# Kernel optimization log

Hardware: AMD Instinct MI355X
Metric: run time of the kernel (lower is better)

The kernel has to match this reference:

```python
import jax, jax.numpy as jnp
import numpy as np
from jax import lax

N, E, F, H, B = 16384, 262144, 32, 128, 16
DI, DS, DC, DTR = 256, 16, 4, 8   # Mamba: d_inner=expand*H, d_state, d_conv, dt_rank=ceil(H/16)
NS, NC = 512, 8                   # num_stations, num line colors
EPS = 1e-5


def _forward(node_features, edge_index, batch, W_in, b_in, W_g1, b_g1, W_g2, b_g2,
             W_inproj, conv_w, conv_b, W_xproj, W_dt, b_dt, A_log, D_p, W_out,
             gamma, beta, Wc, bc, Wh, bh, Wt, bt, Wp1, bp1, Wp2, bp2, Wd, bd, Ws, bs):
    def gcn(x, W, b):
        # GCNConv with self-loops and symmetric normalization
        loops = jnp.arange(N)
        s = jnp.concatenate([edge_index[0], loops])
        d = jnp.concatenate([edge_index[1], loops])
        deg = jax.ops.segment_sum(jnp.ones(s.shape[0], x.dtype), d, num_segments=N)
        dinv = jnp.where(deg > 0, lax.rsqrt(deg), 0.0)
        xw = x @ W
        msg = xw[s] * (dinv[s] * dinv[d])[:, None]
        return jax.ops.segment_sum(msg, d, num_segments=N) + b

    h = jax.nn.relu(node_features @ W_in + b_in)
    h = jax.nn.relu(gcn(h, W_g1, b_g1))
    h_gnn = jax.nn.relu(gcn(h, W_g2, b_g2))

    # --- Mamba block over the node sequence (batch dim of 1, seq_len = N) ---
    xz = h_gnn @ W_inproj                      # (N, 2*DI)
    x, z = xz[:, :DI], xz[:, DI:]
    xp = jnp.pad(x, ((DC - 1, 0), (0, 0)))     # causal depthwise conv1d
    xc = conv_b + sum(xp[k:k + N] * conv_w[:, k] for k in range(DC))
    x = jax.nn.silu(xc)
    dbl = x @ W_xproj                          # (N, DTR + 2*DS)
    dt = jax.nn.softplus(dbl[:, :DTR] @ W_dt + b_dt)   # (N, DI)
    Bm = dbl[:, DTR:DTR + DS]                  # (N, DS)
    Cm = dbl[:, DTR + DS:]                     # (N, DS)
    A = -jnp.exp(A_log)                        # (DI, DS)
    dA = jnp.exp(dt[:, :, None] * A[None])     # (N, DI, DS)
    dBx = dt[:, :, None] * Bm[:, None, :] * x[:, :, None]

    def step(hst, t):
        dA_t, dBx_t, C_t = t
        hst = dA_t * hst + dBx_t               # (DI, DS)
        return hst, hst @ C_t                  # (DI,)

    _, ys = lax.scan(step, jnp.zeros((DI, DS), x.dtype), (dA, dBx, Cm))
    y = (ys + D_p * x) * jax.nn.silu(z)
    h_mamba = y @ W_out                        # (N, H)

    # residual + LayerNorm
    hh = h_gnn + h_mamba
    mu = hh.mean(-1, keepdims=True)
    var = ((hh - mu) ** 2).mean(-1, keepdims=True)
    h_final = (hh - mu) * lax.rsqrt(var + EPS) * gamma + beta

    # global_mean_pool per graph
    counts = jax.ops.segment_sum(jnp.ones(N, h_final.dtype), batch, num_segments=B)
    ge = jax.ops.segment_sum(h_final, batch, num_segments=B) / jnp.maximum(counts, 1.0)[:, None]

    # critic + all policy heads, concatenated: [1,4,3,NS,NS,NS,NC]
    return jnp.concatenate([ge @ Wc + bc, ge @ Wh + bh, ge @ Wt + bt,
                            ge @ Wp1 + bp1, ge @ Wp2 + bp2, ge @ Wd + bd,
                            ge @ Ws + bs], axis=-1)


def setup_inputs() -> dict:
    key = jax.random.key(0)
    ks = list(jax.random.split(key, 20))
    p = lambda i, shape, s=0.02: jax.random.normal(ks[i], shape, jnp.float32) * s
    return dict(
        node_features=jax.random.normal(ks[0], (N, F), jnp.float32),
        edge_index=jax.random.randint(ks[1], (2, E), 0, N),
        batch=jnp.sort(jax.random.randint(ks[2], (N,), 0, B)),
        W_in=p(3, (F, H)), b_in=jnp.zeros((H,), jnp.float32),
        W_g1=p(4, (H, H)), b_g1=jnp.zeros((H,), jnp.float32),
        W_g2=p(5, (H, H)), b_g2=jnp.zeros((H,), jnp.float32),
        W_inproj=p(6, (H, 2 * DI)),
        conv_w=p(7, (DI, DC)), conv_b=jnp.zeros((DI,), jnp.float32),
        W_xproj=p(8, (DI, DTR + 2 * DS)),
        W_dt=p(9, (DTR, DI)), b_dt=jnp.full((DI,), -4.0, jnp.float32),
        A_log=jnp.log(jnp.broadcast_to(jnp.arange(1.0, DS + 1.0, dtype=jnp.float32), (DI, DS))),
        D_p=jnp.ones((DI,), jnp.float32),
        W_out=p(10, (DI, H)),
        gamma=jnp.ones((H,), jnp.float32), beta=jnp.zeros((H,), jnp.float32),
        Wc=p(11, (H, 1)), bc=jnp.zeros((1,), jnp.float32),
        Wh=p(12, (H, 4)), bh=jnp.zeros((4,), jnp.float32),
        Wt=p(13, (H, 3)), bt=jnp.zeros((3,), jnp.float32),
        Wp1=p(14, (H, NS)), bp1=jnp.zeros((NS,), jnp.float32),
        Wp2=p(15, (H, NS)), bp2=jnp.zeros((NS,), jnp.float32),
        Wd=p(16, (H, NS)), bd=jnp.zeros((NS,), jnp.float32),
        Ws=p(17, (H, NC)), bs=jnp.zeros((NC,), jnp.float32),
    )


def reference(node_features, edge_index, batch, W_in, b_in, W_g1, b_g1, W_g2, b_g2,
              W_inproj, conv_w, conv_b, W_xproj, W_dt, b_dt, A_log, D_p, W_out,
              gamma, beta, Wc, bc, Wh, bh, Wt, bt, Wp1, bp1, Wp2, bp2, Wd, bd, Ws, bs):
    return _forward(node_features, edge_index, batch, W_in, b_in, W_g1, b_g1, W_g2, b_g2,
                    W_inproj, conv_w, conv_b, W_xproj, W_dt, b_dt, A_log, D_p, W_out,
                    gamma, beta, Wc, bc, Wh, bh, Wt, bt, Wp1, bp1, Wp2, bp2, Wd, bd, Ws, bs)
```

## Files before the change

kernel.cpp:

```cpp
#include <hip/hip_runtime.h>
#include <math.h>

#define NN 16384
#define EE 262144
#define FF 32
#define HH 128
#define BB 16
#define DI 256
#define DS 16
#define DC 4
#define DTR 8
#define OUTW 1552
#define NCH 256
#define CHLEN 64
#define NG 8
#define GL 32

__device__ __forceinline__ float siluf(float v) { return v / (1.f + __expf(-v)); }
__device__ __forceinline__ float softplusf(float v) {
    return fmaxf(v, 0.f) + __logf(1.f + __expf(-fabsf(v)));
}

__global__ void deg_kernel(const int* __restrict__ dst, int* __restrict__ cnt) {
    int e = blockIdx.x * blockDim.x + threadIdx.x;
    if (e < EE) atomicAdd(&cnt[dst[e]], 1);
}

__global__ __launch_bounds__(1024) void prefix_kernel(const int* __restrict__ cnt,
                                                      int* __restrict__ rowptr,
                                                      int* __restrict__ cursor,
                                                      float* __restrict__ dinv) {
    __shared__ int part[1024];
    int tid = threadIdx.x;
    int4 c4[4];
#pragma unroll
    for (int j = 0; j < 4; j++) c4[j] = ((const int4*)cnt)[tid * 4 + j];
    int v[16] = {c4[0].x, c4[0].y, c4[0].z, c4[0].w, c4[1].x, c4[1].y, c4[1].z, c4[1].w,
                 c4[2].x, c4[2].y, c4[2].z, c4[2].w, c4[3].x, c4[3].y, c4[3].z, c4[3].w};
    int s = 0;
#pragma unroll
    for (int j = 0; j < 16; j++) s += v[j];
    part[tid] = s;
    __syncthreads();
    for (int off = 1; off < 1024; off <<= 1) {
        int t = (tid >= off) ? part[tid - off] : 0;
        __syncthreads();
        part[tid] += t;
        __syncthreads();
    }
    int running = part[tid] - s;
    int rp[16];
    float dv[16];
#pragma unroll
    for (int j = 0; j < 16; j++) {
        rp[j] = running;
        running += v[j];
        dv[j] = rsqrtf((float)(v[j] + 1));
    }
#pragma unroll
    for (int j = 0; j < 4; j++) {
        int4 r4; r4.x = rp[j*4]; r4.y = rp[j*4+1]; r4.z = rp[j*4+2]; r4.w = rp[j*4+3];
        ((int4*)rowptr)[tid * 4 + j] = r4;
        ((int4*)cursor)[tid * 4 + j] = r4;
        float4 d4; d4.x = dv[j*4]; d4.y = dv[j*4+1]; d4.z = dv[j*4+2]; d4.w = dv[j*4+3];
        ((float4*)dinv)[tid * 4 + j] = d4;
    }
    if (tid == 1023) rowptr[NN] = part[1023];
}

__global__ void scatter_kernel(const int* __restrict__ src, const int* __restrict__ dst,
                               int* __restrict__ cursor, int* __restrict__ col) {
    int e = blockIdx.x * blockDim.x + threadIdx.x;
    if (e < EE) {
        int d = dst[e];
        int pos = atomicAdd(&cursor[d], 1);
        col[pos] = src[e];
    }
}

__global__ __launch_bounds__(256) void gemm_k(const float* __restrict__ A,
                                              const float* __restrict__ B,
                                              const float* __restrict__ bias,
                                              float* __restrict__ C,
                                              int M, int Nn, int K, int act) {
    __shared__ float As[16][68];
    __shared__ float Bs[16][68];
    int tid = threadIdx.x;
    int m0 = blockIdx.y * 64;
    int n0 = blockIdx.x * 64;
    int ty = tid >> 4, tx = tid & 15;
    float acc[4][4] = {{0.f}};
    for (int k0 = 0; k0 < K; k0 += 16) {
#pragma unroll
        for (int l = 0; l < 4; l++) {
            int idx = tid + l * 256;
            int i = idx >> 4, j = idx & 15;
            As[j][i] = A[(size_t)(m0 + i) * K + k0 + j];
        }
#pragma unroll
        for (int l = 0; l < 4; l++) {
            int idx = tid + l * 256;
            int i = idx >> 6, j = idx & 63;
            int n = n0 + j;
            Bs[i][j] = (n < Nn) ? B[(size_t)(k0 + i) * Nn + n] : 0.f;
        }
        __syncthreads();
#pragma unroll
        for (int kk = 0; kk < 16; kk++) {
            float4 a4 = *(const float4*)&As[kk][ty * 4];
            float4 b4 = *(const float4*)&Bs[kk][tx * 4];
            float av[4] = {a4.x, a4.y, a4.z, a4.w};
            float bv[4] = {b4.x, b4.y, b4.z, b4.w};
#pragma unroll
            for (int r = 0; r < 4; r++)
#pragma unroll
                for (int c = 0; c < 4; c++) acc[r][c] = fmaf(av[r], bv[c], acc[r][c]);
        }
        __syncthreads();
    }
    int nb = n0 + tx * 4;
    if (nb < Nn) {
        float4 bi4 = {0.f, 0.f, 0.f, 0.f};
        if (bias) bi4 = *(const float4*)&bias[nb];
#pragma unroll
        for (int r = 0; r < 4; r++) {
            int m = m0 + ty * 4 + r;
            float4 v;
            v.x = acc[r][0] + bi4.x; v.y = acc[r][1] + bi4.y;
            v.z = acc[r][2] + bi4.z; v.w = acc[r][3] + bi4.w;
            if (act == 1) {
                v.x = fmaxf(v.x, 0.f); v.y = fmaxf(v.y, 0.f);
                v.z = fmaxf(v.z, 0.f); v.w = fmaxf(v.w, 0.f);
            }
            *(float4*)&C[(size_t)m * Nn + nb] = v;
        }
    }
}

__global__ __launch_bounds__(256, 2) void gemm_big(const float* __restrict__ A,
                                                   const float* __restrict__ B,
                                                   float* __restrict__ C,
                                                   int M, int Nn, int K) {
    __shared__ float As[16][132];
    __shared__ float Bs[16][132];
    int tid = threadIdx.x;
    int m0 = blockIdx.y * 128;
    int n0 = blockIdx.x * 128;
    int ty = tid >> 4, tx = tid & 15;
    float acc[8][8] = {{0.f}};
    for (int k0 = 0; k0 < K; k0 += 16) {
        {
            int m = tid >> 1;
            int kc = (tid & 1) * 8;
            const float* ap = &A[(size_t)(m0 + m) * K + k0 + kc];
            float4 a0 = *(const float4*)ap;
            float4 a1 = *(const float4*)(ap + 4);
            As[kc + 0][m] = a0.x; As[kc + 1][m] = a0.y;
            As[kc + 2][m] = a0.z; As[kc + 3][m] = a0.w;
            As[kc + 4][m] = a1.x; As[kc + 5][m] = a1.y;
            As[kc + 6][m] = a1.z; As[kc + 7][m] = a1.w;
        }
        {
            int krow = tid >> 4;
            int c8 = (tid & 15) * 8;
            const float* bp = &B[(size_t)(k0 + krow) * Nn + n0 + c8];
            *(float4*)&Bs[krow][c8] = *(const float4*)bp;
            *(float4*)&Bs[krow][c8 + 4] = *(const float4*)(bp + 4);
        }
        __syncthreads();
#pragma unroll
        for (int kk = 0; kk < 16; kk++) {
            float4 a0 = *(const float4*)&As[kk][ty * 4];
            float4 a1 = *(const float4*)&As[kk][64 + ty * 4];
            float4 b0 = *(const float4*)&Bs[kk][tx * 4];
            float4 b1 = *(const float4*)&Bs[kk][64 + tx * 4];
            float av[8] = {a0.x, a0.y, a0.z, a0.w, a1.x, a1.y, a1.z, a1.w};
            float bv[8] = {b0.x, b0.y, b0.z, b0.w, b1.x, b1.y, b1.z, b1.w};
#pragma unroll
            for (int r = 0; r < 8; r++)
#pragma unroll
                for (int c = 0; c < 8; c++) acc[r][c] = fmaf(av[r], bv[c], acc[r][c]);
        }
        __syncthreads();
    }
#pragma unroll
    for (int r = 0; r < 8; r++) {
        int m = m0 + ((r < 4) ? (ty * 4 + r) : (64 + ty * 4 + r - 4));
        float4 v0, v1;
        v0.x = acc[r][0]; v0.y = acc[r][1]; v0.z = acc[r][2]; v0.w = acc[r][3];
        v1.x = acc[r][4]; v1.y = acc[r][5]; v1.z = acc[r][6]; v1.w = acc[r][7];
        *(float4*)&C[(size_t)m * Nn + n0 + tx * 4] = v0;
        *(float4*)&C[(size_t)m * Nn + n0 + 64 + tx * 4] = v1;
    }
}

__global__ __launch_bounds__(256) void gemm_at(const float* __restrict__ AT,
                                               const float* __restrict__ B,
                                               float* __restrict__ C,
                                               int M, int Nn, int K) {
    __shared__ float As[16][68];
    __shared__ float Bs[16][68];
    int tid = threadIdx.x;
    int m0 = blockIdx.y * 64;
    int n0 = blockIdx.x * 64;
    int ty = tid >> 4, tx = tid & 15;
    float acc[4][4] = {{0.f}};
    for (int k0 = 0; k0 < K; k0 += 16) {
#pragma unroll
        for (int l = 0; l < 4; l++) {
            int idx = tid + l * 256;
            int kk = idx >> 6, i = idx & 63;
            As[kk][i] = AT[(size_t)(k0 + kk) * M + m0 + i];
        }
#pragma unroll
        for (int l = 0; l < 4; l++) {
            int idx = tid + l * 256;
            int i = idx >> 6, j = idx & 63;
            int n = n0 + j;
            Bs[i][j] = (n < Nn) ? B[(size_t)(k0 + i) * Nn + n] : 0.f;
        }
        __syncthreads();
#pragma unroll
        for (int kk = 0; kk < 16; kk++) {
            float4 a4 = *(const float4*)&As[kk][ty * 4];
            float4 b4 = *(const float4*)&Bs[kk][tx * 4];
            float av[4] = {a4.x, a4.y, a4.z, a4.w};
            float bv[4] = {b4.x, b4.y, b4.z, b4.w};
#pragma unroll
            for (int r = 0; r < 4; r++)
#pragma unroll
                for (int c = 0; c < 4; c++) acc[r][c] = fmaf(av[r], bv[c], acc[r][c]);
        }
        __syncthreads();
    }
    int nb = n0 + tx * 4;
    if (nb < Nn) {
#pragma unroll
        for (int r = 0; r < 4; r++) {
            int m = m0 + ty * 4 + r;
            float4 v;
            v.x = acc[r][0]; v.y = acc[r][1]; v.z = acc[r][2]; v.w = acc[r][3];
            *(float4*)&C[(size_t)m * Nn + nb] = v;
        }
    }
}

__global__ void gcn_gather(const float* __restrict__ xw, const int* __restrict__ rowptr,
                           const int* __restrict__ col, const float* __restrict__ dinv,
                           const float* __restrict__ b, float* __restrict__ out) {
    int n = blockIdx.x;
    int f = threadIdx.x;
    float dn = dinv[n];
    float acc = xw[(size_t)n * HH + f] * dn * dn;
    int beg = rowptr[n], end = rowptr[n + 1];
    int e = beg;
    for (; e + 4 <= end; e += 4) {
        int s0 = col[e], s1 = col[e + 1], s2 = col[e + 2], s3 = col[e + 3];
        float w0 = dinv[s0] * dn, w1 = dinv[s1] * dn, w2 = dinv[s2] * dn, w3 = dinv[s3] * dn;
        float v0 = xw[(size_t)s0 * HH + f];
        float v1 = xw[(size_t)s1 * HH + f];
        float v2 = xw[(size_t)s2 * HH + f];
        float v3 = xw[(size_t)s3 * HH + f];
        acc = fmaf(v0, w0, acc);
        acc = fmaf(v1, w1, acc);
        acc = fmaf(v2, w2, acc);
        acc = fmaf(v3, w3, acc);
    }
    for (; e < end; e++) {
        int s0 = col[e];
        acc = fmaf(xw[(size_t)s0 * HH + f], dinv[s0] * dn, acc);
    }
    acc += b[f];
    out[(size_t)n * HH + f] = fmaxf(acc, 0.f);
}

__global__ __launch_bounds__(256) void conv_silu_t(const float* __restrict__ xz,
                                                   const float* __restrict__ cw,
                                                   const float* __restrict__ cb,
                                                   float* __restrict__ xst,
                                                   float* __restrict__ szt) {
    __shared__ float tile[67][65];
    int tid = threadIdx.x;
    int t0 = blockIdx.x * 64;
    int c0 = blockIdx.y * 64;
#pragma unroll
    for (int l = 0; l < 17; l++) {
        int idx = tid + l * 256;
        if (idx < 67 * 64) {
            int r = idx >> 6, c = idx & 63;
            int gt = t0 - 3 + r;
            tile[r][c] = (gt >= 0) ? xz[(size_t)gt * 512 + c0 + c] : 0.f;
        }
    }
    __syncthreads();
    int tl = tid & 63;
    int d0 = tid >> 6;
    if (c0 < 256) {
#pragma unroll
        for (int l = 0; l < 16; l++) {
            int dl = d0 + l * 4;
            int dg = c0 + dl;
            float acc = cb[dg];
#pragma unroll
            for (int k = 0; k < DC; k++)
                acc = fmaf(tile[tl + k][dl], cw[dg * DC + k], acc);
            xst[dg * NN + t0 + tl] = siluf(acc);
        }
    } else {
#pragma unroll
        for (int l = 0; l < 16; l++) {
            int dl = d0 + l * 4;
            int dg = c0 - 256 + dl;
            szt[dg * NN + t0 + tl] = siluf(tile[tl + 3][dl]);
        }
    }
}

__global__ __launch_bounds__(256) void transpose_dbl(const float* __restrict__ dbl,
                                                     float* __restrict__ dblt) {
    __shared__ float tile[64][41];
    int tid = threadIdx.x;
    int t0 = blockIdx.x * 64;
#pragma unroll
    for (int l = 0; l < 10; l++) {
        int idx = tid + l * 256;
        int r = idx / 40, c = idx - r * 40;
        tile[r][c] = dbl[(size_t)(t0 + r) * 40 + c];
    }
    __syncthreads();
#pragma unroll
    for (int l = 0; l < 10; l++) {
        int idx = tid + l * 256;
        int c = idx >> 6, t = idx & 63;
        dblt[c * NN + t0 + t] = tile[t][c];
    }
}

__global__ __launch_bounds__(256, 6) void scan_phase1(const float* __restrict__ xst,
                                                      const float* __restrict__ dblt,
                                                      const float* __restrict__ A_log,
                                                      const float* __restrict__ W_dt,
                                                      const float* __restrict__ b_dt,
                                                      float* __restrict__ chkP,
                                                      float* __restrict__ chkH) {
    __shared__ float Td[32][68];
    __shared__ float Tx[32][68];
    __shared__ float Bs[16][68];
    __shared__ float D8[8][68];
    int tid = threadIdx.x;
    int wave = tid >> 6, lane = tid & 63;
    int sg = lane & 7, dl = lane >> 3;
    int dblk = blockIdx.x, chunk = blockIdx.y;
    int t0 = chunk * CHLEN;
    int dloc = wave * 8 + dl;
    int d = dblk * 32 + dloc;
    int s0 = 2 * sg;
#pragma unroll
    for (int p = 0; p < 2; p++) {
        int linear = tid + p * 256;
        int row = linear >> 4, c4 = (linear & 15) * 4;
        *(float4*)&Tx[row][c4] = *(const float4*)&xst[(size_t)(dblk * 32 + row) * NN + t0 + c4];
    }
    if (tid < 128) {
        int r = tid >> 4, c4 = (tid & 15) * 4;
        *(float4*)&D8[r][c4] = *(const float4*)&dblt[(size_t)r * NN + t0 + c4];
    }
    {
        int s = tid >> 4, c4 = (tid & 15) * 4;
        *(float4*)&Bs[s][c4] = *(const float4*)&dblt[(size_t)(8 + s) * NN + t0 + c4];
    }
    float A0 = -expf(A_log[d * DS + s0]);
    float A1 = -expf(A_log[d * DS + s0 + 1]);
    __syncthreads();
    {
        int row = tid >> 3;
        int tb = (tid & 7) * 8;
        int dd = dblk * 32 + row;
        float bd = b_dt[dd];
        float wv[8];
#pragma unroll
        for (int j = 0; j < 8; j++) wv[j] = W_dt[j * DI + dd];
#pragma unroll
        for (int j = 0; j < 8; j++) {
            int t = tb + j;
            float acc = bd;
#pragma unroll
            for (int k = 0; k < 8; k++) acc = fmaf(D8[k][t], wv[k], acc);
            Td[row][t] = softplusf(acc);
        }
    }
    __syncthreads();
    float h0 = 0.f, h1 = 0.f, P0 = 1.f, P1 = 1.f;
    for (int i = 0; i < CHLEN; i += 4) {
        float4 d4 = *(const float4*)&Td[dloc][i];
        float4 x4 = *(const float4*)&Tx[dloc][i];
        float4 b04 = *(const float4*)&Bs[s0][i];
        float4 b14 = *(const float4*)&Bs[s0 + 1][i];
#define P1S(U) { float dtv = d4.U; float a0 = __expf(dtv * A0); float a1 = __expf(dtv * A1); \
        float dx = dtv * x4.U; h0 = fmaf(a0, h0, dx * b04.U); h1 = fmaf(a1, h1, dx * b14.U); \
        P0 *= a0; P1 *= a1; }
        P1S(x) P1S(y) P1S(z) P1S(w)
#undef P1S
    }
    int idx = chunk * 4096 + d * DS + s0;
    float2 vP; vP.x = P0; vP.y = P1;
    float2 vH; vH.x = h0; vH.y = h1;
    *(float2*)(chkP + idx) = vP;
    *(float2*)(chkH + idx) = vH;
}

__global__ void scan_phase2a(const float* __restrict__ chkP, const float* __restrict__ chkH,
                             float* __restrict__ gp, float* __restrict__ gh) {
    int g = blockIdx.x * blockDim.x + threadIdx.x;
    int idx = g & 4095;
    int grp = g >> 12;
    int c0 = grp * GL;
    float P = 1.f, H = 0.f;
    for (int j = 0; j < GL; j += 4) {
        float p[4], q[4];
#pragma unroll
        for (int jj = 0; jj < 4; jj++) {
            p[jj] = chkP[(c0 + j + jj) * 4096 + idx];
            q[jj] = chkH[(c0 + j + jj) * 4096 + idx];
        }
#pragma unroll
        for (int jj = 0; jj < 4; jj++) {
            H = fmaf(p[jj], H, q[jj]);
            P *= p[jj];
        }
    }
    gp[grp * 4096 + idx] = P;
    gh[grp * 4096 + idx] = H;
}

__global__ void scan_phase2b(const float* __restrict__ gp, const float* __restrict__ gh,
                             float* __restrict__ gini) {
    int idx = blockIdx.x * blockDim.x + threadIdx.x;
    float h = 0.f;
#pragma unroll
    for (int g = 0; g < NG; g++) {
        gini[g * 4096 + idx] = h;
        h = fmaf(gp[g * 4096 + idx], h, gh[g * 4096 + idx]);
    }
}

__global__ void scan_phase2c(const float* __restrict__ chkP, const float* __restrict__ chkH,
                             const float* __restrict__ gini, float* __restrict__ init) {
    int g = blockIdx.x * blockDim.x + threadIdx.x;
    int idx = g & 4095;
    int grp = g >> 12;
    int c0 = grp * GL;
    float h = gini[grp * 4096 + idx];
    for (int j = 0; j < GL; j += 4) {
        float p[4], q[4];
#pragma unroll
        for (int jj = 0; jj < 4; jj++) {
            p[jj] = chkP[(c0 + j + jj) * 4096 + idx];
            q[jj] = chkH[(c0 + j + jj) * 4096 + idx];
        }
#pragma unroll
        for (int jj = 0; jj < 4; jj++) {
            init[(c0 + j + jj) * 4096 + idx] = h;
            h = fmaf(p[jj], h, q[jj]);
        }
    }
}

__global__ __launch_bounds__(256, 5) void scan_phase3(const float* __restrict__ xst,
                                                      const float* __restrict__ dblt,
                                                      const float* __restrict__ A_log,
                                                      const float* __restrict__ W_dt,
                                                      const float* __restrict__ b_dt,
                                                      const float* __restrict__ init,
                                                      const float* __restrict__ D_p,
                                                      const float* __restrict__ szt,
                                                      float* __restrict__ yt) {
    __shared__ float Td[32][68];
    __shared__ float Tx[32][68];
    __shared__ float Bs[16][68];
    __shared__ float Cs[16][68];
    __shared__ float D8[8][68];
    int tid = threadIdx.x;
    int wave = tid >> 6, lane = tid & 63;
    int sg = lane & 7, dl = lane >> 3;
    int dblk = blockIdx.x, chunk = blockIdx.y;
    int t0 = chunk * CHLEN;
    int dloc = wave * 8 + dl;
    int d = dblk * 32 + dloc;
    int s0 = 2 * sg;
#pragma unroll
    for (int p = 0; p < 2; p++) {
        int linear = tid + p * 256;
        int row = linear >> 4, c4 = (linear & 15) * 4;
        *(float4*)&Tx[row][c4] = *(const float4*)&xst[(size_t)(dblk * 32 + row) * NN + t0 + c4];
    }
    if (tid < 128) {
        int r = tid >> 4, c4 = (tid & 15) * 4;
        *(float4*)&D8[r][c4] = *(const float4*)&dblt[(size_t)r * NN + t0 + c4];
    }
    {
        int s = tid >> 4, c4 = (tid & 15) * 4;
        *(float4*)&Bs[s][c4] = *(const float4*)&dblt[(size_t)(8 + s) * NN + t0 + c4];
        *(float4*)&Cs[s][c4] = *(const float4*)&dblt[(size_t)(24 + s) * NN + t0 + c4];
    }
    float A0 = -expf(A_log[d * DS + s0]);
    float A1 = -expf(A_log[d * DS + s0 + 1]);
    float Dd = D_p[d];
    float2 ini = *(const float2*)(init + chunk * 4096 + d * DS + s0);
    float h0 = ini.x, h1 = ini.y;
    __syncthreads();
    {
        int row = tid >> 3;
        int tb = (tid & 7) * 8;
        int dd = dblk * 32 + row;
        float bd = b_dt[dd];
        float wv[8];
#pragma unroll
        for (int j = 0; j < 8; j++) wv[j] = W_dt[j * DI + dd];
#pragma unroll
        for (int j = 0; j < 8; j++) {
            int t = tb + j;
            float acc = bd;
#pragma unroll
            for (int k = 0; k < 8; k++) acc = fmaf(D8[k][t], wv[k], acc);
            Td[row][t] = softplusf(acc);
        }
    }
    __syncthreads();
    for (int i = 0; i < CHLEN; i += 4) {
        float4 d4 = *(const float4*)&Td[dloc][i];
        float4 x4 = *(const float4*)&Tx[dloc][i];
        float4 b04 = *(const float4*)&Bs[s0][i];
        float4 b14 = *(const float4*)&Bs[s0 + 1][i];
        float4 c04 = *(const float4*)&Cs[s0][i];
        float4 c14 = *(const float4*)&Cs[s0 + 1][i];
        float4 yv;
#define P3S(U) { float dtv = d4.U; float a0 = __expf(dtv * A0); float a1 = __expf(dtv * A1); \
        float dx = dtv * x4.U; h0 = fmaf(a0, h0, dx * b04.U); h1 = fmaf(a1, h1, dx * b14.U); \
        float c = fmaf(h1, c14.U, h0 * c04.U); \
        c += __shfl_xor(c, 1); c += __shfl_xor(c, 2); c += __shfl_xor(c, 4); \
        yv.U = c + Dd * x4.U; }
        P3S(x) P3S(y) P3S(z) P3S(w)
#undef P3S
        if (sg == 0) *(float4*)&Td[dloc][i] = yv;
    }
#pragma unroll
    for (int r = 0; r < 8; r++) {
        int row = wave * 8 + r;
        float sz = szt[(size_t)(dblk * 32 + row) * NN + t0 + lane];
        yt[(size_t)(dblk * 32 + row) * NN + t0 + lane] = Td[row][lane] * sz;
    }
}

__global__ void add_ln(const float* __restrict__ hg, const float* __restrict__ hm,
                       const float* __restrict__ gamma, const float* __restrict__ beta,
                       float* __restrict__ out) {
    int row = blockIdx.x * 4 + (threadIdx.x >> 6);
    int lane = threadIdx.x & 63;
    size_t base = (size_t)row * HH;
    float v0 = hg[base + lane] + hm[base + lane];
    float v1 = hg[base + 64 + lane] + hm[base + 64 + lane];
    float sum = v0 + v1;
#pragma unroll
    for (int m = 32; m >= 1; m >>= 1) sum += __shfl_xor(sum, m);
    float mu = sum * (1.f / 128.f);
    float d0 = v0 - mu, d1 = v1 - mu;
    float vs = d0 * d0 + d1 * d1;
#pragma unroll
    for (int m = 32; m >= 1; m >>= 1) vs += __shfl_xor(vs, m);
    float inv = rsqrtf(vs * (1.f / 128.f) + 1e-5f);
    out[base + lane] = d0 * inv * gamma[lane] + beta[lane];
    out[base + 64 + lane] = d1 * inv * gamma[64 + lane] + beta[64 + lane];
}

__global__ void pool_kernel(const float* __restrict__ hf, const int* __restrict__ batch,
                            float* __restrict__ ge, int* __restrict__ counts) {
    int f = threadIdx.x;
    int r0 = blockIdx.x * 128;
    int gcur = batch[r0];
    float acc = 0.f;
    int cnt = 0;
    for (int i = 0; i < 128; i += 4) {
        int r = r0 + i;
        int g0 = batch[r], g3 = batch[r + 3];
        float v0 = hf[(size_t)r * HH + f];
        float v1 = hf[(size_t)(r + 1) * HH + f];
        float v2 = hf[(size_t)(r + 2) * HH + f];
        float v3 = hf[(size_t)(r + 3) * HH + f];
        if (g0 == gcur && g3 == gcur) {
            acc += (v0 + v1) + (v2 + v3);
            cnt += 4;
        } else {
            int gs[4] = {g0, batch[r + 1], batch[r + 2], g3};
            float vs[4] = {v0, v1, v2, v3};
#pragma unroll
            for (int k = 0; k < 4; k++) {
                if (gs[k] != gcur) {
                    atomicAdd(&ge[gcur * HH + f], acc);
                    if (f == 0) atomicAdd(&counts[gcur], cnt);
                    acc = 0.f; cnt = 0; gcur = gs[k];
                }
                acc += vs[k];
                cnt++;
            }
        }
    }
    atomicAdd(&ge[gcur * HH + f], acc);
    if (f == 0) atomicAdd(&counts[gcur], cnt);
}

__global__ void ge_norm(float* __restrict__ ge, const int* __restrict__ counts) {
    int idx = blockIdx.x * blockDim.x + threadIdx.x;
    if (idx < BB * HH) {
        int b = idx >> 7;
        ge[idx] /= fmaxf((float)counts[b], 1.f);
    }
}

__global__ void heads_kernel(const float* __restrict__ ge,
                             const float* Wc, const float* bc, const float* Wh, const float* bh,
                             const float* Wt, const float* bt, const float* Wp1, const float* bp1,
                             const float* Wp2, const float* bp2, const float* Wd, const float* bd,
                             const float* Ws, const float* bs, float* __restrict__ out) {
    int col = blockIdx.x * blockDim.x + threadIdx.x;
    int b = blockIdx.y;
    if (col >= OUTW) return;
    const float* W; const float* bi; int lc, w;
    if (col < 1)         { W = Wc;  bi = bc;  lc = col;        w = 1; }
    else if (col < 5)    { W = Wh;  bi = bh;  lc = col - 1;    w = 4; }
    else if (col < 8)    { W = Wt;  bi = bt;  lc = col - 5;    w = 3; }
    else if (col < 520)  { W = Wp1; bi = bp1; lc = col - 8;    w = 512; }
    else if (col < 1032) { W = Wp2; bi = bp2; lc = col - 520;  w = 512; }
    else if (col < 1544) { W = Wd;  bi = bd;  lc = col - 1032; w = 512; }
    else                 { W = Ws;  bi = bs;  lc = col - 1544; w = 8; }
    float acc = bi[lc];
#pragma unroll 8
    for (int f = 0; f < HH; f++) acc = fmaf(ge[b * HH + f], W[f * w + lc], acc);
    out[(size_t)b * OUTW + col] = acc;
}

extern "C" void kernel_launch(void* const* d_in, const int* in_sizes, int n_in,
                              void* d_out, int out_size, void* d_ws, size_t ws_size,
                              hipStream_t stream) {
    const float* nf      = (const float*)d_in[0];
    const int*   ei      = (const int*)d_in[1];
    const int*   batch   = (const int*)d_in[2];
    const float* W_in    = (const float*)d_in[3];
    const float* b_in    = (const float*)d_in[4];
    const float* W_g1    = (const float*)d_in[5];
    const float* b_g1    = (const float*)d_in[6];
    const float* W_g2    = (const float*)d_in[7];
    const float* b_g2    = (const float*)d_in[8];
    const float* W_inproj= (const float*)d_in[9];
    const float* conv_w  = (const float*)d_in[10];
    const float* conv_b  = (const float*)d_in[11];
    const float* W_xproj = (const float*)d_in[12];
    const float* W_dt    = (const float*)d_in[13];
    const float* b_dt    = (const float*)d_in[14];
    const float* A_log   = (const float*)d_in[15];
    const float* D_p     = (const float*)d_in[16];
    const float* W_out   = (const float*)d_in[17];
    const float* gamma   = (const float*)d_in[18];
    const float* beta    = (const float*)d_in[19];
    const float* Wc = (const float*)d_in[20]; const float* bc = (const float*)d_in[21];
    const float* Wh = (const float*)d_in[22]; const float* bh = (const float*)d_in[23];
    const float* Wt = (const float*)d_in[24]; const float* bt = (const float*)d_in[25];
    const float* Wp1= (const float*)d_in[26]; const float* bp1= (const float*)d_in[27];
    const float* Wp2= (const float*)d_in[28]; const float* bp2= (const float*)d_in[29];
    const float* Wd = (const float*)d_in[30]; const float* bd = (const float*)d_in[31];
    const float* Ws = (const float*)d_in[32]; const float* bs = (const float*)d_in[33];

    const int* e_src = ei;
    const int* e_dst = ei + EE;

    float* w = (float*)d_ws;
    size_t o = 0;
    float* F0   = w + o; o += (size_t)NN * HH;
    float* F1   = w + o; o += (size_t)NN * HH;
    float* F2   = w + o; o += (size_t)NN * HH;
    float* XZ   = w + o; o += (size_t)NN * 512;
    float* YT   = XZ;
    float* XST  = w + o; o += (size_t)NN * DI;
    float* SZT  = w + o; o += (size_t)NN * DI;
    float* DBL  = w + o; o += (size_t)NN * 40;
    float* DBLT = w + o; o += (size_t)NN * 40;
    float* GE   = w + o; o += BB * HH;
    float* DINV = w + o; o += NN;
    int* ip = (int*)(w + o);
    int* CNT    = ip; ip += NN;
    int* ROWPTR = ip; ip += NN + 1;
    int* CURSOR = ip; ip += NN;
    int* COL    = ip; ip += EE;
    int* COUNTS = ip; ip += BB;

    float* CHP  = F0;
    float* CHH  = F0 + (size_t)NCH * 4096;
    float* INI  = F1;
    float* GP   = DBL;
    float* GH   = DBL + NG * 4096;
    float* GINI = DBL + 2 * NG * 4096;

    hipMemsetAsync(CNT, 0, NN * sizeof(int), stream);
    hipMemsetAsync(GE, 0, BB * HH * sizeof(float), stream);
    hipMemsetAsync(COUNTS, 0, BB * sizeof(int), stream);

    deg_kernel<<<EE / 256, 256, 0, stream>>>(e_dst, CNT);
    prefix_kernel<<<1, 1024, 0, stream>>>(CNT, ROWPTR, CURSOR, DINV);
    scatter_kernel<<<EE / 256, 256, 0, stream>>>(e_src, e_dst, CURSOR, COL);

    gemm_k<<<dim3(2, NN / 64), 256, 0, stream>>>(nf, W_in, b_in, F0, NN, HH, FF, 1);
    gemm_k<<<dim3(2, NN / 64), 256, 0, stream>>>(F0, W_g1, nullptr, F1, NN, HH, HH, 0);
    gcn_gather<<<NN, HH, 0, stream>>>(F1, ROWPTR, COL, DINV, b_g1, F0);
    gemm_k<<<dim3(2, NN / 64), 256, 0, stream>>>(F0, W_g2, nullptr, F1, NN, HH, HH, 0);
    gcn_gather<<<NN, HH, 0, stream>>>(F1, ROWPTR, COL, DINV, b_g2, F2);

    gemm_big<<<dim3(4, NN / 128), 256, 0, stream>>>(F2, W_inproj, XZ, NN, 512, HH);
    conv_silu_t<<<dim3(NN / 64, 8), 256, 0, stream>>>(XZ, conv_w, conv_b, XST, SZT);
    gemm_at<<<dim3(1, NN / 64), 256, 0, stream>>>(XST, W_xproj, DBL, NN, 40, DI);
    transpose_dbl<<<NN / 64, 256, 0, stream>>>(DBL, DBLT);

    scan_phase1<<<dim3(8, NCH), 256, 0, stream>>>(XST, DBLT, A_log, W_dt, b_dt, CHP, CHH);
    scan_phase2a<<<(4096 * NG) / 256, 256, 0, stream>>>(CHP, CHH, GP, GH);
    scan_phase2b<<<16, 256, 0, stream>>>(GP, GH, GINI);
    scan_phase2c<<<(4096 * NG) / 256, 256, 0, stream>>>(CHP, CHH, GINI, INI);
    scan_phase3<<<dim3(8, NCH), 256, 0, stream>>>(XST, DBLT, A_log, W_dt, b_dt, INI, D_p, SZT, YT);

    gemm_at<<<dim3(2, NN / 64), 256, 0, stream>>>(YT, W_out, F1, NN, HH, DI);
    add_ln<<<NN / 4, 256, 0, stream>>>(F2, F1, gamma, beta, F0);

    pool_kernel<<<NN / 128, HH, 0, stream>>>(F0, batch, GE, COUNTS);
    ge_norm<<<(BB * HH + 255) / 256, 256, 0, stream>>>(GE, COUNTS);

    heads_kernel<<<dim3((OUTW + 127) / 128, BB), 128, 0, stream>>>(
        GE, Wc, bc, Wh, bh, Wt, bt, Wp1, bp1, Wp2, bp2, Wd, bd, Ws, bs, (float*)d_out);
}
```

Before: 449.0 us.

## Fuse out-proj GEMM with residual LayerNorm, vectorize GCN gather, fold pool normalization

```diff
diff --git a/kernel.cpp b/kernel.cpp
--- a/kernel.cpp
+++ b/kernel.cpp
@@ -137,7 +137,7 @@
     }
 }
 
-__global__ __launch_bounds__(256, 2) void gemm_big(const float* __restrict__ A,
+__global__ __launch_bounds__(256, 4) void gemm_big(const float* __restrict__ A,
                                                    const float* __restrict__ B,
                                                    float* __restrict__ C,
                                                    int M, int Nn, int K) {
@@ -245,33 +245,126 @@
     }
 }
 
-__global__ void gcn_gather(const float* __restrict__ xw, const int* __restrict__ rowptr,
-                           const int* __restrict__ col, const float* __restrict__ dinv,
-                           const float* __restrict__ b, float* __restrict__ out) {
-    int n = blockIdx.x;
-    int f = threadIdx.x;
+__global__ __launch_bounds__(256) void gemm_at_ln(const float* __restrict__ AT,
+                                                  const float* __restrict__ B,
+                                                  const float* __restrict__ hg,
+                                                  const float* __restrict__ gamma,
+                                                  const float* __restrict__ beta,
+                                                  float* __restrict__ out) {
+    __shared__ float As[16][68];
+    __shared__ float Bs[16][132];
+    int tid = threadIdx.x;
+    int m0 = blockIdx.x * 64;
+    int ty = tid >> 4, tx = tid & 15;
+    float acc[4][8] = {{0.f}};
+    for (int k0 = 0; k0 < 256; k0 += 16) {
+#pragma unroll
+        for (int l = 0; l < 4; l++) {
+            int idx = tid + l * 256;
+            int kk = idx >> 6, i = idx & 63;
+            As[kk][i] = AT[(size_t)(k0 + kk) * NN + m0 + i];
+        }
+        {
+            int krow = tid >> 4;
+            int c8 = (tid & 15) * 8;
+            const float* bp = &B[(size_t)(k0 + krow) * HH + c8];
+            *(float4*)&Bs[krow][c8] = *(const float4*)bp;
+            *(float4*)&Bs[krow][c8 + 4] = *(const float4*)(bp + 4);
+        }
+        __syncthreads();
+#pragma unroll
+        for (int kk = 0; kk < 16; kk++) {
+            float4 a4 = *(const float4*)&As[kk][ty * 4];
+            float4 b0 = *(const float4*)&Bs[kk][tx * 4];
+            float4 b1 = *(const float4*)&Bs[kk][64 + tx * 4];
+            float av[4] = {a4.x, a4.y, a4.z, a4.w};
+            float bv[8] = {b0.x, b0.y, b0.z, b0.w, b1.x, b1.y, b1.z, b1.w};
+#pragma unroll
+            for (int r = 0; r < 4; r++)
+#pragma unroll
+                for (int c = 0; c < 8; c++) acc[r][c] = fmaf(av[r], bv[c], acc[r][c]);
+        }
+        __syncthreads();
+    }
+    float4 g0 = *(const float4*)&gamma[tx * 4];
+    float4 g1 = *(const float4*)&gamma[64 + tx * 4];
+    float4 be0 = *(const float4*)&beta[tx * 4];
+    float4 be1 = *(const float4*)&beta[64 + tx * 4];
+    float gv[8] = {g0.x, g0.y, g0.z, g0.w, g1.x, g1.y, g1.z, g1.w};
+    float bv[8] = {be0.x, be0.y, be0.z, be0.w, be1.x, be1.y, be1.z, be1.w};
+#pragma unroll
+    for (int r = 0; r < 4; r++) {
+        int m = m0 + ty * 4 + r;
+        float4 h0 = *(const float4*)&hg[(size_t)m * HH + tx * 4];
+        float4 h1 = *(const float4*)&hg[(size_t)m * HH + 64 + tx * 4];
+        float v[8] = {acc[r][0] + h0.x, acc[r][1] + h0.y, acc[r][2] + h0.z, acc[r][3] + h0.w,
+                      acc[r][4] + h1.x, acc[r][5] + h1.y, acc[r][6] + h1.z, acc[r][7] + h1.w};
+        float sum = 0.f;
+#pragma unroll
+        for (int c = 0; c < 8; c++) sum += v[c];
+        sum += __shfl_xor(sum, 1); sum += __shfl_xor(sum, 2);
+        sum += __shfl_xor(sum, 4); sum += __shfl_xor(sum, 8);
+        float mu = sum * (1.f / 128.f);
+        float vs = 0.f;
+#pragma unroll
+        for (int c = 0; c < 8; c++) { float dd = v[c] - mu; vs += dd * dd; }
+        vs += __shfl_xor(vs, 1); vs += __shfl_xor(vs, 2);
+        vs += __shfl_xor(vs, 4); vs += __shfl_xor(vs, 8);
+        float inv = rsqrtf(vs * (1.f / 128.f) + 1e-5f);
+        float4 o0, o1;
+        o0.x = (v[0] - mu) * inv * gv[0] + bv[0];
+        o0.y = (v[1] - mu) * inv * gv[1] + bv[1];
+        o0.z = (v[2] - mu) * inv * gv[2] + bv[2];
+        o0.w = (v[3] - mu) * inv * gv[3] + bv[3];
+        o1.x = (v[4] - mu) * inv * gv[4] + bv[4];
+        o1.y = (v[5] - mu) * inv * gv[5] + bv[5];
+        o1.z = (v[6] - mu) * inv * gv[6] + bv[6];
+        o1.w = (v[7] - mu) * inv * gv[7] + bv[7];
+        *(float4*)&out[(size_t)m * HH + tx * 4] = o0;
+        *(float4*)&out[(size_t)m * HH + 64 + tx * 4] = o1;
+    }
+}
+
+__global__ __launch_bounds__(256) void gcn_gather4(const float* __restrict__ xw,
+                                                   const int* __restrict__ rowptr,
+                                                   const int* __restrict__ col,
+                                                   const float* __restrict__ dinv,
+                                                   const float* __restrict__ b,
+                                                   float* __restrict__ out) {
+    int tid = threadIdx.x;
+    int sub = tid & 31;
+    int n = blockIdx.x * 8 + (tid >> 5);
     float dn = dinv[n];
-    float acc = xw[(size_t)n * HH + f] * dn * dn;
+    const float4* xw4 = (const float4*)xw;
+    float4 a = xw4[(size_t)n * 32 + sub];
+    float ws = dn * dn;
+    float4 acc;
+    acc.x = a.x * ws; acc.y = a.y * ws; acc.z = a.z * ws; acc.w = a.w * ws;
     int beg = rowptr[n], end = rowptr[n + 1];
     int e = beg;
-    for (; e + 4 <= end; e += 4) {
-        int s0 = col[e], s1 = col[e + 1], s2 = col[e + 2], s3 = col[e + 3];
-        float w0 = dinv[s0] * dn, w1 = dinv[s1] * dn, w2 = dinv[s2] * dn, w3 = dinv[s3] * dn;
-        float v0 = xw[(size_t)s0 * HH + f];
-        float v1 = xw[(size_t)s1 * HH + f];
-        float v2 = xw[(size_t)s2 * HH + f];
-        float v3 = xw[(size_t)s3 * HH + f];
-        acc = fmaf(v0, w0, acc);
-        acc = fmaf(v1, w1, acc);
-        acc = fmaf(v2, w2, acc);
-        acc = fmaf(v3, w3, acc);
-    }
-    for (; e < end; e++) {
+    for (; e + 2 <= end; e += 2) {
+        int s0 = col[e], s1 = col[e + 1];
+        float w0 = dinv[s0] * dn, w1 = dinv[s1] * dn;
+        float4 v0 = xw4[(size_t)s0 * 32 + sub];
+        float4 v1 = xw4[(size_t)s1 * 32 + sub];
+        acc.x = fmaf(v0.x, w0, acc.x); acc.y = fmaf(v0.y, w0, acc.y);
+        acc.z = fmaf(v0.z, w0, acc.z); acc.w = fmaf(v0.w, w0, acc.w);
+        acc.x = fmaf(v1.x, w1, acc.x); acc.y = fmaf(v1.y, w1, acc.y);
+        acc.z = fmaf(v1.z, w1, acc.z); acc.w = fmaf(v1.w, w1, acc.w);
+    }
+    if (e < end) {
         int s0 = col[e];
-        acc = fmaf(xw[(size_t)s0 * HH + f], dinv[s0] * dn, acc);
-    }
-    acc += b[f];
-    out[(size_t)n * HH + f] = fmaxf(acc, 0.f);
+        float w0 = dinv[s0] * dn;
+        float4 v0 = xw4[(size_t)s0 * 32 + sub];
+        acc.x = fmaf(v0.x, w0, acc.x); acc.y = fmaf(v0.y, w0, acc.y);
+        acc.z = fmaf(v0.z, w0, acc.z); acc.w = fmaf(v0.w, w0, acc.w);
+    }
+    float4 b4 = ((const float4*)b)[sub];
+    acc.x = fmaxf(acc.x + b4.x, 0.f);
+    acc.y = fmaxf(acc.y + b4.y, 0.f);
+    acc.z = fmaxf(acc.z + b4.z, 0.f);
+    acc.w = fmaxf(acc.w + b4.w, 0.f);
+    ((float4*)out)[(size_t)n * 32 + sub] = acc;
 }
 
 __global__ __launch_bounds__(256) void conv_silu_t(const float* __restrict__ xz,
@@ -550,27 +643,6 @@
         float sz = szt[(size_t)(dblk * 32 + row) * NN + t0 + lane];
         yt[(size_t)(dblk * 32 + row) * NN + t0 + lane] = Td[row][lane] * sz;
     }
-}
-
-__global__ void add_ln(const float* __restrict__ hg, const float* __restrict__ hm,
-                       const float* __restrict__ gamma, const float* __restrict__ beta,
-                       float* __restrict__ out) {
-    int row = blockIdx.x * 4 + (threadIdx.x >> 6);
-    int lane = threadIdx.x & 63;
-    size_t base = (size_t)row * HH;
-    float v0 = hg[base + lane] + hm[base + lane];
-    float v1 = hg[base + 64 + lane] + hm[base + 64 + lane];
-    float sum = v0 + v1;
-#pragma unroll
-    for (int m = 32; m >= 1; m >>= 1) sum += __shfl_xor(sum, m);
-    float mu = sum * (1.f / 128.f);
-    float d0 = v0 - mu, d1 = v1 - mu;
-    float vs = d0 * d0 + d1 * d1;
-#pragma unroll
-    for (int m = 32; m >= 1; m >>= 1) vs += __shfl_xor(vs, m);
-    float inv = rsqrtf(vs * (1.f / 128.f) + 1e-5f);
-    out[base + lane] = d0 * inv * gamma[lane] + beta[lane];
-    out[base + 64 + lane] = d1 * inv * gamma[64 + lane] + beta[64 + lane];
 }
 
 __global__ void pool_kernel(const float* __restrict__ hf, const int* __restrict__ batch,
@@ -609,15 +681,7 @@
     if (f == 0) atomicAdd(&counts[gcur], cnt);
 }
 
-__global__ void ge_norm(float* __restrict__ ge, const int* __restrict__ counts) {
-    int idx = blockIdx.x * blockDim.x + threadIdx.x;
-    if (idx < BB * HH) {
-        int b = idx >> 7;
-        ge[idx] /= fmaxf((float)counts[b], 1.f);
-    }
-}
-
-__global__ void heads_kernel(const float* __restrict__ ge,
+__global__ void heads_kernel(const float* __restrict__ ge, const int* __restrict__ counts,
                              const float* Wc, const float* bc, const float* Wh, const float* bh,
                              const float* Wt, const float* bt, const float* Wp1, const float* bp1,
                              const float* Wp2, const float* bp2, const float* Wd, const float* bd,
@@ -633,10 +697,11 @@
     else if (col < 1032) { W = Wp2; bi = bp2; lc = col - 520;  w = 512; }
     else if (col < 1544) { W = Wd;  bi = bd;  lc = col - 1032; w = 512; }
     else                 { W = Ws;  bi = bs;  lc = col - 1544; w = 8; }
-    float acc = bi[lc];
+    float scale = 1.f / fmaxf((float)counts[b], 1.f);
+    float dot = 0.f;
 #pragma unroll 8
-    for (int f = 0; f < HH; f++) acc = fmaf(ge[b * HH + f], W[f * w + lc], acc);
-    out[(size_t)b * OUTW + col] = acc;
+    for (int f = 0; f < HH; f++) dot = fmaf(ge[b * HH + f], W[f * w + lc], dot);
+    out[(size_t)b * OUTW + col] = bi[lc] + scale * dot;
 }
 
 extern "C" void kernel_launch(void* const* d_in, const int* in_sizes, int n_in,
@@ -710,9 +775,9 @@
 
     gemm_k<<<dim3(2, NN / 64), 256, 0, stream>>>(nf, W_in, b_in, F0, NN, HH, FF, 1);
     gemm_k<<<dim3(2, NN / 64), 256, 0, stream>>>(F0, W_g1, nullptr, F1, NN, HH, HH, 0);
-    gcn_gather<<<NN, HH, 0, stream>>>(F1, ROWPTR, COL, DINV, b_g1, F0);
+    gcn_gather4<<<NN / 8, 256, 0, stream>>>(F1, ROWPTR, COL, DINV, b_g1, F0);
     gemm_k<<<dim3(2, NN / 64), 256, 0, stream>>>(F0, W_g2, nullptr, F1, NN, HH, HH, 0);
-    gcn_gather<<<NN, HH, 0, stream>>>(F1, ROWPTR, COL, DINV, b_g2, F2);
+    gcn_gather4<<<NN / 8, 256, 0, stream>>>(F1, ROWPTR, COL, DINV, b_g2, F2);
 
     gemm_big<<<dim3(4, NN / 128), 256, 0, stream>>>(F2, W_inproj, XZ, NN, 512, HH);
     conv_silu_t<<<dim3(NN / 64, 8), 256, 0, stream>>>(XZ, conv_w, conv_b, XST, SZT);
@@ -725,12 +790,10 @@
     scan_phase2c<<<(4096 * NG) / 256, 256, 0, stream>>>(CHP, CHH, GINI, INI);
     scan_phase3<<<dim3(8, NCH), 256, 0, stream>>>(XST, DBLT, A_log, W_dt, b_dt, INI, D_p, SZT, YT);
 
-    gemm_at<<<dim3(2, NN / 64), 256, 0, stream>>>(YT, W_out, F1, NN, HH, DI);
-    add_ln<<<NN / 4, 256, 0, stream>>>(F2, F1, gamma, beta, F0);
+    gemm_at_ln<<<NN / 64, 256, 0, stream>>>(YT, W_out, F2, gamma, beta, F0);
 
     pool_kernel<<<NN / 128, HH, 0, stream>>>(F0, batch, GE, COUNTS);
-    ge_norm<<<(BB * HH + 255) / 256, 256, 0, stream>>>(GE, COUNTS);
 
     heads_kernel<<<dim3((OUTW + 127) / 128, BB), 128, 0, stream>>>(
-        GE, Wc, bc, Wh, bh, Wt, bt, Wp1, bp1, Wp2, bp2, Wd, bd, Ws, bs, (float*)d_out);
-}
+        GE, COUNTS, Wc, bc, Wh, bh, Wt, bt, Wp1, bp1, Wp2, bp2, Wd, bd, Ws, bs, (float*)d_out);
+}
```

Measured after the change: 425.3 us. 1.06x faster.
